# Kernel tuning notes

Hardware: AMD Instinct MI355X
Metric: run time of the kernel (lower is better)

## Reference

```python
import jax, jax.numpy as jnp
import numpy as np
from jax import lax

T, L, K = 1024, 32, 128
BEG = 0  # index of '[BEG]' in the label dict


def setup_inputs() -> dict:
    key = jax.random.key(0)
    kx, kw, kl = jax.random.split(key, 3)
    X = jax.random.normal(kx, (T, L, L, K), dtype=jnp.float32)
    w = jax.random.normal(kw, (K,), dtype=jnp.float32)  # nn.Parameter, init N(0,1)
    label = jax.random.randint(kl, (T,), 0, L, dtype=jnp.int32)
    return {"X": X, "w": w, "label": label}


def reference(X, w, label):
    """CRF negative log-likelihood (forward algorithm over log-potential matrices)."""
    # Ms[t, i, j] = log-potential of transition i->j at step t  (X @ w)
    Ms = jnp.einsum('tijk,k->tij', X, w)  # [T, L, L]

    # forward recurrence: alpha_t[j] = logsumexp_i(alpha_{t-1}[i] + Ms[t, i, j])
    alpha0 = Ms[0, BEG, :]  # [L]

    def step(alpha, M):
        new = jax.nn.logsumexp(alpha[:, None] + M, axis=0)
        return new, None

    alpha_last, _ = lax.scan(step, alpha0, Ms[1:])
    logZ = jax.nn.logsumexp(alpha_last)

    # gold-path score: sum_t Ms[t, prev_label_t, label_t], prev_0 = BEG
    prev = jnp.concatenate([jnp.array([BEG], dtype=label.dtype), label[:-1]])
    t_idx = jnp.arange(Ms.shape[0])
    path_score = jnp.sum(Ms[t_idx, prev, label])

    return -path_score + logZ
```

## Files before the change

### kernel.cpp

```cpp
#include <hip/hip_runtime.h>

#define TT 1024
#define LL 32
#define LDP (LL + 1)
#define CHUNK 4
#define NBLK (TT / CHUNK)

#define ALPHA0_OFF 0
#define PATH_OFF   32
#define P0_OFF     288
#define P1_OFF     (P0_OFF + 256 * 1024)
#define P2_OFF     (P1_OFF + 64 * 1024)
#define P3_OFF     (P2_OFF + 16 * 1024)
#define CNT_OFF    (P3_OFF + 4 * 1024)

__device__ __forceinline__ float lse_mul_step(float a, const float* Bcol) {
  float s[LL];
  #pragma unroll
  for (int k = 0; k < LL; k++) s[k] = __shfl(a, k, 32) + Bcol[k * LDP];
  float t[16];
  #pragma unroll
  for (int k = 0; k < 16; k++) t[k] = fmaxf(s[k], s[k + 16]);
  #pragma unroll
  for (int st = 8; st >= 1; st >>= 1) {
    #pragma unroll
    for (int k = 0; k < st; k++) t[k] = fmaxf(t[k], t[k + st]);
  }
  const float mx = t[0];
  float a0 = 0.f, a1 = 0.f, a2 = 0.f, a3 = 0.f;
  #pragma unroll
  for (int k = 0; k < LL; k += 4) {
    a0 += __expf(s[k]     - mx);
    a1 += __expf(s[k + 1] - mx);
    a2 += __expf(s[k + 2] - mx);
    a3 += __expf(s[k + 3] - mx);
  }
  return mx + __logf((a0 + a1) + (a2 + a3));
}

__global__ __launch_bounds__(1024, 1) void crf_fused(
    const float4* __restrict__ X4, const float* __restrict__ w,
    const int* __restrict__ label, float* __restrict__ ws,
    int* __restrict__ cnt, float* __restrict__ out) {
  __shared__ float Ms[CHUNK][LL][LDP];
  __shared__ float M4[4][LL][LDP];
  __shared__ float redm[16], reds[16], redp[16];
  __shared__ int last;
  const int blk = blockIdx.x, tid = threadIdx.x;
  const int l5 = tid & 31;
  const int grp = tid >> 5;
  const float4 w4 = reinterpret_cast<const float4*>(w)[l5];
  const size_t base = (size_t)blk * CHUNK * 1024u * 32u;

  #pragma unroll
  for (int m = 0; m < CHUNK; m++) {
    #pragma unroll 4
    for (int it = 0; it < LL; it++) {
      float4 xv = X4[base + (size_t)(m * 1024 + it * 32 + grp) * 32u + l5];
      float v = fmaf(xv.x, w4.x, fmaf(xv.y, w4.y, fmaf(xv.z, w4.z, xv.w * w4.w)));
      v += __shfl_xor(v, 16, 32);
      v += __shfl_xor(v,  8, 32);
      v += __shfl_xor(v,  4, 32);
      v += __shfl_xor(v,  2, 32);
      v += __shfl_xor(v,  1, 32);
      if (l5 == 0) Ms[m][it][grp] = v;
    }
  }
  __syncthreads();

  if (tid == 0) {
    float ps = 0.f;
    const int t0 = blk * CHUNK;
    for (int m = 0; m < CHUNK; m++) {
      const int t = t0 + m;
      const int lab = label[t];
      const int pv = (t == 0) ? 0 : label[t - 1];
      ps += Ms[m][pv][lab];
    }
    ws[PATH_OFF + blk] = ps;
  }
  if (blk == 0 && tid < LL) ws[ALPHA0_OFF + tid] = Ms[0][0][tid];

  const int i2 = tid >> 5, j2 = tid & 31;
  const int first = (blk == 0) ? 1 : 0;
  float a = Ms[first][i2][j2];
  #pragma unroll
  for (int m = 1; m < CHUNK; m++)
    if (m > first) a = lse_mul_step(a, &Ms[m][0][j2]);

  const int POFF[4] = {P0_OFF, P1_OFF, P2_OFF, P3_OFF};
  const int CB[4]   = {0, 64, 80, 84};
  int idx = blk;
  for (int lvl = 0; lvl < 4; lvl++) {
    ws[POFF[lvl] + (size_t)idx * 1024 + tid] = a;
    __syncthreads();
    if (tid == 0) {
      __threadfence();
      last = atomicAdd(&cnt[CB[lvl] + (idx >> 2)], 1);
    }
    __syncthreads();
    if (last != 3) return;
    if (tid == 0) __threadfence();
    __syncthreads();
    const int g = idx >> 2;
    const float* sp = ws + POFF[lvl] + (size_t)g * 4 * 1024;
    #pragma unroll
    for (int r = 0; r < 4; r++) M4[r][i2][j2] = sp[(size_t)r * 1024 + tid];
    __syncthreads();
    a = M4[0][i2][j2];
    #pragma unroll
    for (int r = 1; r < 4; r++) a = lse_mul_step(a, &M4[r][0][j2]);
    idx = g;
  }

  const float v = ws[ALPHA0_OFF + i2] + a;
  float mx = v;
  #pragma unroll
  for (int o = 32; o >= 1; o >>= 1) mx = fmaxf(mx, __shfl_xor(mx, o));
  const int wid = tid >> 6, lane = tid & 63;
  if (lane == 0) redm[wid] = mx;
  __syncthreads();
  float mb = redm[0];
  #pragma unroll
  for (int q = 1; q < 16; q++) mb = fmaxf(mb, redm[q]);
  float e = __expf(v - mb);
  float p = (tid < 256) ? ws[PATH_OFF + tid] : 0.f;
  #pragma unroll
  for (int o = 32; o >= 1; o >>= 1) {
    e += __shfl_xor(e, o);
    p += __shfl_xor(p, o);
  }
  if (lane == 0) { reds[wid] = e; redp[wid] = p; }
  __syncthreads();
  if (tid == 0) {
    float s = 0.f, ps = 0.f;
    for (int q = 0; q < 16; q++) { s += reds[q]; ps += redp[q]; }
    out[0] = -ps + (mb + __logf(s));
  }
}

extern "C" void kernel_launch(void* const* d_in, const int* in_sizes, int n_in,
                              void* d_out, int out_size, void* d_ws, size_t ws_size,
                              hipStream_t stream) {
  const float4* X4 = (const float4*)d_in[0];
  const float* w = (const float*)d_in[1];
  const int* label = (const int*)d_in[2];
  float* out = (float*)d_out;
  float* ws = (float*)d_ws;
  int* cnt = (int*)(ws + CNT_OFF);

  hipMemsetAsync(cnt, 0, 85 * sizeof(int), stream);
  crf_fused<<<NBLK, 1024, 0, stream>>>(X4, w, label, ws, cnt, out);
}
```

Measured before the change: 164.9 us.

## Split fused CRF kernel into GEMV, tree-reduction, and final kernels

After: 187.8 us. 1.14x slower.

```diff
diff --git a/kernel.cpp b/kernel.cpp
--- a/kernel.cpp
+++ b/kernel.cpp
@@ -1,18 +1,12 @@
 #include <hip/hip_runtime.h>
 
+#define LL 32
+#define LDP 33
 #define TT 1024
-#define LL 32
-#define LDP (LL + 1)
-#define CHUNK 4
-#define NBLK (TT / CHUNK)
 
-#define ALPHA0_OFF 0
-#define PATH_OFF   32
-#define P0_OFF     288
-#define P1_OFF     (P0_OFF + 256 * 1024)
-#define P2_OFF     (P1_OFF + 64 * 1024)
-#define P3_OFF     (P2_OFF + 16 * 1024)
-#define CNT_OFF    (P3_OFF + 4 * 1024)
+#define MS_OFF 0
+#define P0_OFF (MS_OFF + TT * 1024)
+#define P1_OFF (P0_OFF + 128 * 1024)
 
 __device__ __forceinline__ float lse_mul_step(float a, const float* Bcol) {
   float s[LL];
@@ -38,82 +32,93 @@
   return mx + __logf((a0 + a1) + (a2 + a3));
 }
 
-__global__ __launch_bounds__(1024, 1) void crf_fused(
-    const float4* __restrict__ X4, const float* __restrict__ w,
-    const int* __restrict__ label, float* __restrict__ ws,
-    int* __restrict__ cnt, float* __restrict__ out) {
-  __shared__ float Ms[CHUNK][LL][LDP];
-  __shared__ float M4[4][LL][LDP];
-  __shared__ float redm[16], reds[16], redp[16];
-  __shared__ int last;
-  const int blk = blockIdx.x, tid = threadIdx.x;
-  const int l5 = tid & 31;
-  const int grp = tid >> 5;
-  const float4 w4 = reinterpret_cast<const float4*>(w)[l5];
-  const size_t base = (size_t)blk * CHUNK * 1024u * 32u;
-
+template <int R>
+__device__ __forceinline__ float lse_tree(float (*S)[LL][LDP], int i, int j, bool id0) {
+  float c[R / 2];
   #pragma unroll
-  for (int m = 0; m < CHUNK; m++) {
-    #pragma unroll 4
-    for (int it = 0; it < LL; it++) {
-      float4 xv = X4[base + (size_t)(m * 1024 + it * 32 + grp) * 32u + l5];
-      float v = fmaf(xv.x, w4.x, fmaf(xv.y, w4.y, fmaf(xv.z, w4.z, xv.w * w4.w)));
-      v += __shfl_xor(v, 16, 32);
-      v += __shfl_xor(v,  8, 32);
-      v += __shfl_xor(v,  4, 32);
-      v += __shfl_xor(v,  2, 32);
-      v += __shfl_xor(v,  1, 32);
-      if (l5 == 0) Ms[m][it][grp] = v;
+  for (int p = 0; p < R / 2; p++) {
+    float a = (p == 0 && id0) ? ((i == j) ? 0.f : -1e30f) : S[2 * p][i][j];
+    c[p] = lse_mul_step(a, &S[2 * p + 1][0][j]);
+    __builtin_amdgcn_sched_barrier(0);
+  }
+  #pragma unroll
+  for (int n = R / 2; n > 1; n >>= 1) {
+    __syncthreads();
+    #pragma unroll
+    for (int q = 0; q < n / 2; q++) S[2 * q + 1][i][j] = c[2 * q + 1];
+    __syncthreads();
+    #pragma unroll
+    for (int q = 0; q < n / 2; q++) {
+      c[q] = lse_mul_step(c[2 * q], &S[2 * q + 1][0][j]);
+      __builtin_amdgcn_sched_barrier(0);
     }
   }
+  return c[0];
+}
+
+__global__ __launch_bounds__(256) void crf_gemv(
+    const float4* __restrict__ X4, const float* __restrict__ w,
+    float* __restrict__ ms) {
+  __shared__ float sm[512];
+  const int tid = threadIdx.x, l5 = tid & 31, g = tid >> 5;
+  const float4 w4 = reinterpret_cast<const float4*>(w)[l5];
+  const size_t cbase = (size_t)blockIdx.x * 512;
+  const float4* xp = X4 + cbase * 32;
+  #pragma unroll 8
+  for (int it = 0; it < 64; it++) {
+    const int cell = it * 8 + g;
+    const float4 xv = xp[cell * 32 + l5];
+    float v = fmaf(xv.x, w4.x, fmaf(xv.y, w4.y, fmaf(xv.z, w4.z, xv.w * w4.w)));
+    v += __shfl_xor(v, 16, 32);
+    v += __shfl_xor(v,  8, 32);
+    v += __shfl_xor(v,  4, 32);
+    v += __shfl_xor(v,  2, 32);
+    v += __shfl_xor(v,  1, 32);
+    if (l5 == 0) sm[cell] = v;
+  }
   __syncthreads();
+  if (tid < 128)
+    reinterpret_cast<float4*>(ms + cbase)[tid] = reinterpret_cast<const float4*>(sm)[tid];
+}
 
-  if (tid == 0) {
-    float ps = 0.f;
-    const int t0 = blk * CHUNK;
-    for (int m = 0; m < CHUNK; m++) {
-      const int t = t0 + m;
-      const int lab = label[t];
-      const int pv = (t == 0) ? 0 : label[t - 1];
-      ps += Ms[m][pv][lab];
-    }
-    ws[PATH_OFF + blk] = ps;
-  }
-  if (blk == 0 && tid < LL) ws[ALPHA0_OFF + tid] = Ms[0][0][tid];
+__global__ __launch_bounds__(1024, 1) void crf_leaf8(
+    const float* __restrict__ ms, float* __restrict__ p0) {
+  __shared__ float S[8][LL][LDP];
+  const int blk = blockIdx.x, tid = threadIdx.x;
+  const int i = tid >> 5, j = tid & 31;
+  #pragma unroll
+  for (int m = 0; m < 8; m++) S[m][i][j] = ms[((size_t)blk * 8 + m) * 1024 + tid];
+  __syncthreads();
+  const float r = lse_tree<8>(S, i, j, blk == 0);
+  p0[(size_t)blk * 1024 + tid] = r;
+}
 
-  const int i2 = tid >> 5, j2 = tid & 31;
-  const int first = (blk == 0) ? 1 : 0;
-  float a = Ms[first][i2][j2];
+__global__ __launch_bounds__(1024, 1) void crf_comb16(
+    const float* __restrict__ src, float* __restrict__ dst) {
+  __shared__ float S[16][LL][LDP];
+  const int blk = blockIdx.x, tid = threadIdx.x;
+  const int i = tid >> 5, j = tid & 31;
   #pragma unroll
-  for (int m = 1; m < CHUNK; m++)
-    if (m > first) a = lse_mul_step(a, &Ms[m][0][j2]);
+  for (int m = 0; m < 16; m++) S[m][i][j] = src[((size_t)blk * 16 + m) * 1024 + tid];
+  __syncthreads();
+  const float r = lse_tree<16>(S, i, j, false);
+  dst[(size_t)blk * 1024 + tid] = r;
+}
 
-  const int POFF[4] = {P0_OFF, P1_OFF, P2_OFF, P3_OFF};
-  const int CB[4]   = {0, 64, 80, 84};
-  int idx = blk;
-  for (int lvl = 0; lvl < 4; lvl++) {
-    ws[POFF[lvl] + (size_t)idx * 1024 + tid] = a;
-    __syncthreads();
-    if (tid == 0) {
-      __threadfence();
-      last = atomicAdd(&cnt[CB[lvl] + (idx >> 2)], 1);
-    }
-    __syncthreads();
-    if (last != 3) return;
-    if (tid == 0) __threadfence();
-    __syncthreads();
-    const int g = idx >> 2;
-    const float* sp = ws + POFF[lvl] + (size_t)g * 4 * 1024;
-    #pragma unroll
-    for (int r = 0; r < 4; r++) M4[r][i2][j2] = sp[(size_t)r * 1024 + tid];
-    __syncthreads();
-    a = M4[0][i2][j2];
-    #pragma unroll
-    for (int r = 1; r < 4; r++) a = lse_mul_step(a, &M4[r][0][j2]);
-    idx = g;
-  }
-
-  const float v = ws[ALPHA0_OFF + i2] + a;
+__global__ __launch_bounds__(1024, 1) void crf_final(
+    const float* __restrict__ ws, const int* __restrict__ label,
+    float* __restrict__ out) {
+  __shared__ float S[8][LL][LDP];
+  __shared__ float redm[16], reds[16], redp[16];
+  const int tid = threadIdx.x, i = tid >> 5, j = tid & 31;
+  #pragma unroll
+  for (int m = 0; m < 8; m++) S[m][i][j] = ws[P1_OFF + m * 1024 + tid];
+  __syncthreads();
+  const float a = lse_tree<8>(S, i, j, false);
+  const float v = ws[MS_OFF + i] + a;
+  const int lab = label[tid];
+  const int pv = (tid == 0) ? 0 : label[tid - 1];
+  const float pval = ws[MS_OFF + (size_t)tid * 1024 + pv * 32 + lab];
   float mx = v;
   #pragma unroll
   for (int o = 32; o >= 1; o >>= 1) mx = fmaxf(mx, __shfl_xor(mx, o));
@@ -124,7 +129,7 @@
   #pragma unroll
   for (int q = 1; q < 16; q++) mb = fmaxf(mb, redm[q]);
   float e = __expf(v - mb);
-  float p = (tid < 256) ? ws[PATH_OFF + tid] : 0.f;
+  float p = pval;
   #pragma unroll
   for (int o = 32; o >= 1; o >>= 1) {
     e += __shfl_xor(e, o);
@@ -147,8 +152,9 @@
   const int* label = (const int*)d_in[2];
   float* out = (float*)d_out;
   float* ws = (float*)d_ws;
-  int* cnt = (int*)(ws + CNT_OFF);
 
-  hipMemsetAsync(cnt, 0, 85 * sizeof(int), stream);
-  crf_fused<<<NBLK, 1024, 0, stream>>>(X4, w, label, ws, cnt, out);
+  crf_gemv<<<2048, 256, 0, stream>>>(X4, w, ws + MS_OFF);
+  crf_leaf8<<<128, 1024, 0, stream>>>(ws + MS_OFF, ws + P0_OFF);
+  crf_comb16<<<8, 1024, 0, stream>>>(ws + P0_OFF, ws + P1_OFF);
+  crf_final<<<1, 1024, 0, stream>>>(ws, label, out);
 }
```

## Replace atomic tree reduction with multi-kernel LSE matrix-product tree

Applied to the files above, without the earlier changes.

New measurement: 156.4 us. -5.2%, faster.

```diff
diff --git a/kernel.cpp b/kernel.cpp
--- a/kernel.cpp
+++ b/kernel.cpp
@@ -2,22 +2,21 @@
 
 #define TT 1024
 #define LL 32
-#define LDP (LL + 1)
 #define CHUNK 4
 #define NBLK (TT / CHUNK)
 
 #define ALPHA0_OFF 0
 #define PATH_OFF   32
 #define P0_OFF     288
-#define P1_OFF     (P0_OFF + 256 * 1024)
-#define P2_OFF     (P1_OFF + 64 * 1024)
-#define P3_OFF     (P2_OFF + 16 * 1024)
-#define CNT_OFF    (P3_OFF + 4 * 1024)
+#define Q1_OFF     (P0_OFF + 256 * 1024)
+#define Q2_OFF     (Q1_OFF + 32 * 1024)
 
-__device__ __forceinline__ float lse_mul_step(float a, const float* Bcol) {
+__device__ __forceinline__ float lse_cell(const float A[LL][LL + 1],
+                                          const float B[LL][LL + 1],
+                                          int i, int j) {
   float s[LL];
   #pragma unroll
-  for (int k = 0; k < LL; k++) s[k] = __shfl(a, k, 32) + Bcol[k * LDP];
+  for (int k = 0; k < LL; k++) s[k] = A[i][k] + B[k][j];
   float t[16];
   #pragma unroll
   for (int k = 0; k < 16; k++) t[k] = fmaxf(s[k], s[k + 16]);
@@ -38,39 +37,38 @@
   return mx + __logf((a0 + a1) + (a2 + a3));
 }
 
-__global__ __launch_bounds__(1024, 1) void crf_fused(
+__global__ __launch_bounds__(1024, 1) void crf_stageA(
     const float4* __restrict__ X4, const float* __restrict__ w,
-    const int* __restrict__ label, float* __restrict__ ws,
-    int* __restrict__ cnt, float* __restrict__ out) {
-  __shared__ float Ms[CHUNK][LL][LDP];
-  __shared__ float M4[4][LL][LDP];
-  __shared__ float redm[16], reds[16], redp[16];
-  __shared__ int last;
+    const int* __restrict__ label, float* __restrict__ ws) {
+  __shared__ float Ms[CHUNK][LL][LL + 1];
+  __shared__ float Pb[2][LL][LL + 1];
   const int blk = blockIdx.x, tid = threadIdx.x;
   const int l5 = tid & 31;
-  const int grp = tid >> 5;
+  const int half = (tid >> 5) & 1;
+  const int wid = tid >> 6;
+  const int cellbase = wid * 2 + half;
   const float4 w4 = reinterpret_cast<const float4*>(w)[l5];
-  const size_t base = (size_t)blk * CHUNK * 1024u * 32u;
+  const int t0 = blk * CHUNK;
 
   #pragma unroll
   for (int m = 0; m < CHUNK; m++) {
-    #pragma unroll 4
+    #pragma unroll 8
     for (int it = 0; it < LL; it++) {
-      float4 xv = X4[base + (size_t)(m * 1024 + it * 32 + grp) * 32u + l5];
+      const int cell = it * LL + cellbase;
+      float4 xv = X4[(size_t)(t0 + m) * 1024u * 32u + (size_t)cell * 32u + l5];
       float v = fmaf(xv.x, w4.x, fmaf(xv.y, w4.y, fmaf(xv.z, w4.z, xv.w * w4.w)));
       v += __shfl_xor(v, 16, 32);
       v += __shfl_xor(v,  8, 32);
       v += __shfl_xor(v,  4, 32);
       v += __shfl_xor(v,  2, 32);
       v += __shfl_xor(v,  1, 32);
-      if (l5 == 0) Ms[m][it][grp] = v;
+      if (l5 == 0) Ms[m][it][cellbase] = v;
     }
   }
   __syncthreads();
 
   if (tid == 0) {
     float ps = 0.f;
-    const int t0 = blk * CHUNK;
     for (int m = 0; m < CHUNK; m++) {
       const int t = t0 + m;
       const int lab = label[t];
@@ -81,44 +79,59 @@
   }
   if (blk == 0 && tid < LL) ws[ALPHA0_OFF + tid] = Ms[0][0][tid];
 
-  const int i2 = tid >> 5, j2 = tid & 31;
+  const int i = tid >> 5, j = tid & 31;
   const int first = (blk == 0) ? 1 : 0;
-  float a = Ms[first][i2][j2];
+  Pb[0][i][j] = lse_cell(Ms[first], Ms[first + 1], i, j);
+  int cur = 0;
+  for (int m = first + 2; m < CHUNK; m++) {
+    __syncthreads();
+    float r = lse_cell(Pb[cur], Ms[m], i, j);
+    Pb[cur ^ 1][i][j] = r;
+    cur ^= 1;
+  }
+  ws[P0_OFF + blk * 1024 + tid] = Pb[cur][i][j];
+}
+
+__global__ __launch_bounds__(1024, 1) void crf_comb8(
+    const float* __restrict__ src, float* __restrict__ dst) {
+  __shared__ float S[8][LL][LL + 1];
+  __shared__ float PQ[4][LL][LL + 1];
+  const int blk = blockIdx.x, tid = threadIdx.x;
+  const int i = tid >> 5, j = tid & 31;
   #pragma unroll
-  for (int m = 1; m < CHUNK; m++)
-    if (m > first) a = lse_mul_step(a, &Ms[m][0][j2]);
+  for (int m = 0; m < 8; m++)
+    S[m][i][j] = src[((size_t)blk * 8 + m) * 1024 + tid];
+  __syncthreads();
+  #pragma unroll
+  for (int q = 0; q < 4; q++)
+    PQ[q][i][j] = lse_cell(S[2 * q], S[2 * q + 1], i, j);
+  __syncthreads();
+  S[0][i][j] = lse_cell(PQ[0], PQ[1], i, j);
+  S[1][i][j] = lse_cell(PQ[2], PQ[3], i, j);
+  __syncthreads();
+  dst[(size_t)blk * 1024 + tid] = lse_cell(S[0], S[1], i, j);
+}
 
-  const int POFF[4] = {P0_OFF, P1_OFF, P2_OFF, P3_OFF};
-  const int CB[4]   = {0, 64, 80, 84};
-  int idx = blk;
-  for (int lvl = 0; lvl < 4; lvl++) {
-    ws[POFF[lvl] + (size_t)idx * 1024 + tid] = a;
-    __syncthreads();
-    if (tid == 0) {
-      __threadfence();
-      last = atomicAdd(&cnt[CB[lvl] + (idx >> 2)], 1);
-    }
-    __syncthreads();
-    if (last != 3) return;
-    if (tid == 0) __threadfence();
-    __syncthreads();
-    const int g = idx >> 2;
-    const float* sp = ws + POFF[lvl] + (size_t)g * 4 * 1024;
-    #pragma unroll
-    for (int r = 0; r < 4; r++) M4[r][i2][j2] = sp[(size_t)r * 1024 + tid];
-    __syncthreads();
-    a = M4[0][i2][j2];
-    #pragma unroll
-    for (int r = 1; r < 4; r++) a = lse_mul_step(a, &M4[r][0][j2]);
-    idx = g;
-  }
+__global__ __launch_bounds__(1024, 1) void crf_final4(
+    const float* __restrict__ ws, float* __restrict__ out) {
+  __shared__ float S[4][LL][LL + 1];
+  __shared__ float PQ[2][LL][LL + 1];
+  __shared__ float redm[16], reds[16], redp[16];
+  const int tid = threadIdx.x, i = tid >> 5, j = tid & 31;
+  #pragma unroll
+  for (int m = 0; m < 4; m++) S[m][i][j] = ws[Q2_OFF + m * 1024 + tid];
+  __syncthreads();
+  PQ[0][i][j] = lse_cell(S[0], S[1], i, j);
+  PQ[1][i][j] = lse_cell(S[2], S[3], i, j);
+  __syncthreads();
+  const float a = lse_cell(PQ[0], PQ[1], i, j);
+  const float v = ws[ALPHA0_OFF + i] + a;
 
-  const float v = ws[ALPHA0_OFF + i2] + a;
   float mx = v;
   #pragma unroll
   for (int o = 32; o >= 1; o >>= 1) mx = fmaxf(mx, __shfl_xor(mx, o));
-  const int wid = tid >> 6, lane = tid & 63;
-  if (lane == 0) redm[wid] = mx;
+  const int wv = tid >> 6, lane = tid & 63;
+  if (lane == 0) redm[wv] = mx;
   __syncthreads();
   float mb = redm[0];
   #pragma unroll
@@ -130,7 +143,7 @@
     e += __shfl_xor(e, o);
     p += __shfl_xor(p, o);
   }
-  if (lane == 0) { reds[wid] = e; redp[wid] = p; }
+  if (lane == 0) { reds[wv] = e; redp[wv] = p; }
   __syncthreads();
   if (tid == 0) {
     float s = 0.f, ps = 0.f;
@@ -147,8 +160,9 @@
   const int* label = (const int*)d_in[2];
   float* out = (float*)d_out;
   float* ws = (float*)d_ws;
-  int* cnt = (int*)(ws + CNT_OFF);
 
-  hipMemsetAsync(cnt, 0, 85 * sizeof(int), stream);
-  crf_fused<<<NBLK, 1024, 0, stream>>>(X4, w, label, ws, cnt, out);
+  crf_stageA<<<NBLK, 1024, 0, stream>>>(X4, w, label, ws);
+  crf_comb8<<<32, 1024, 0, stream>>>(ws + P0_OFF, ws + Q1_OFF);
+  crf_comb8<<<4, 1024, 0, stream>>>(ws + Q1_OFF, ws + Q2_OFF);
+  crf_final4<<<1, 1024, 0, stream>>>(ws, out);
 }
```
